# Optimization experiments

Measured on AMD Instinct MI355X. Metric: run time of the kernel, lower is better.

Reference implementation:

```python
import jax, jax.numpy as jnp
import numpy as np

N_NODES = 100000
N_EDGES = 1600000
F_IN = 128
H = 128
L = 3
BN_EPS = 1e-5
NORM_EPS = 1e-12


def setup_inputs() -> dict:
    key = jax.random.key(0)
    ks = jax.random.split(key, 32)
    def rn(k, shape, s=0.05):
        return jax.random.normal(k, shape, dtype=jnp.float32) * s
    inp = {
        'x': jax.random.normal(ks[0], (N_NODES, F_IN), dtype=jnp.float32),
        'edge_index': jax.random.randint(ks[1], (2, N_EDGES), 0, N_NODES, dtype=jnp.int32),
        # node encoder
        'enc_w': rn(ks[2], (H, F_IN)), 'enc_b': rn(ks[3], (H,)),
        # per-layer SAGEConv params (stacked over layers)
        'lin_l_w': rn(ks[4], (L, H, H)), 'lin_l_b': rn(ks[5], (L, H)),
        'lin_r_w': rn(ks[6], (L, H, H)),
        # batch norms (eval mode: running stats)
        'bn_gamma': jnp.ones((L, H), jnp.float32), 'bn_beta': jnp.zeros((L, H), jnp.float32),
        'bn_mean': jnp.zeros((L, H), jnp.float32), 'bn_var': jnp.ones((L, H), jnp.float32),
        # output head
        'out_w1': rn(ks[7], (H, H)), 'out_b1': rn(ks[8], (H,)),
        'out_w2': rn(ks[9], (1, H)), 'out_b2': rn(ks[10], (1,)),
        # cost head
        'cost_w1': rn(ks[11], (H // 2, H)), 'cost_b1': rn(ks[12], (H // 2,)),
        'cost_w2': rn(ks[13], (1, H // 2)), 'cost_b2': rn(ks[14], (1,)),
        # bullwhip head
        'bw_w1': rn(ks[15], (H // 2, H)), 'bw_b1': rn(ks[16], (H // 2,)),
        'bw_w2': rn(ks[17], (1, H // 2)), 'bw_b2': rn(ks[18], (1,)),
    }
    return inp


def _sage_conv(h, src, dst, wl, bl, wr):
    # PyG SAGEConv (aggr='mean', normalize=True): lin_l(mean_j x_j) + lin_r(x_i), then L2 normalize
    msg_sum = jax.ops.segment_sum(h[src], dst, num_segments=N_NODES)  # [N, H]
    deg = jax.ops.segment_sum(jnp.ones((src.shape[0],), h.dtype), dst, num_segments=N_NODES)
    mean = msg_sum / jnp.maximum(deg, 1.0)[:, None]
    out = mean @ wl.T + bl + h @ wr.T
    norm = jnp.linalg.norm(out, axis=-1, keepdims=True)
    return out / jnp.maximum(norm, NORM_EPS)


def reference(x, edge_index, enc_w, enc_b, lin_l_w, lin_l_b, lin_r_w,
              bn_gamma, bn_beta, bn_mean, bn_var,
              out_w1, out_b1, out_w2, out_b2,
              cost_w1, cost_b1, cost_w2, cost_b2,
              bw_w1, bw_b1, bw_w2, bw_b2):
    src, dst = edge_index[0], edge_index[1]
    h = jax.nn.relu(x @ enc_w.T + enc_b)  # dropout is identity in eval
    for i in range(L):
        h = _sage_conv(h, src, dst, lin_l_w[i], lin_l_b[i], lin_r_w[i])
        # BatchNorm1d in eval mode
        h = (h - bn_mean[i]) * (bn_gamma[i] / jnp.sqrt(bn_var[i] + BN_EPS)) + bn_beta[i]
        h = jax.nn.relu(h)
    order = jax.nn.relu(h @ out_w1.T + out_b1) @ out_w2.T + out_b2
    cost = jax.nn.relu(h @ cost_w1.T + cost_b1) @ cost_w2.T + cost_b2
    bullwhip = jax.nn.relu(h @ bw_w1.T + bw_b1) @ bw_w2.T + bw_b2
    return (order, cost, bullwhip, h)
```

## Files before the change

### kernel.cpp

```cpp
#include <hip/hip_runtime.h>

#define NN 100000
#define NE 1600000
#define TN 16
#define TNL 32
#define NBK 391
#define BCAP 5120
#define CTILE 8192

static constexpr float BN_EPS = 1e-5f;
static constexpr float NORM_EPS = 1e-12f;

typedef unsigned int u32;
typedef unsigned short u16;
typedef __attribute__((ext_vector_type(8))) short short8;
typedef __attribute__((ext_vector_type(4))) float f32x4;

__device__ __forceinline__ float bflo(u32 u) {
    u32 v = u << 16; float f; __builtin_memcpy(&f, &v, 4); return f;
}
__device__ __forceinline__ float bfhi(u32 u) {
    u32 v = u & 0xffff0000u; float f; __builtin_memcpy(&f, &v, 4); return f;
}
__device__ __forceinline__ u32 packbf(float a, float b) {
    u32 ua, ub; __builtin_memcpy(&ua, &a, 4); __builtin_memcpy(&ub, &b, 4);
    u32 ra = (ua + 0x7fffu + ((ua >> 16) & 1u)) >> 16;
    u32 rb = (ub + 0x7fffu + ((ub >> 16) & 1u)) & 0xffff0000u;
    return ra | rb;
}
__device__ __forceinline__ u16 f2bf(float a) {
    u32 ua; __builtin_memcpy(&ua, &a, 4);
    return (u16)((ua + 0x7fffu + ((ua >> 16) & 1u)) >> 16);
}
__device__ __forceinline__ void acc8(float* s, uint4 v) {
    s[0] += bflo(v.x); s[1] += bfhi(v.x);
    s[2] += bflo(v.y); s[3] += bfhi(v.y);
    s[4] += bflo(v.z); s[5] += bfhi(v.z);
    s[6] += bflo(v.w); s[7] += bfhi(v.w);
}
__device__ __forceinline__ f32x4 mfma16(uint4 a, uint4 b, f32x4 c) {
    return __builtin_amdgcn_mfma_f32_16x16x32_bf16(
        __builtin_bit_cast(short8, a), __builtin_bit_cast(short8, b), c, 0, 0, 0);
}

struct TposeArgs {
    const float* src[10];
    u16* dst[10];
    int rows[10];
};

__global__ void frag_kernel(TposeArgs a) {
    const int m = blockIdx.x;
    const float* __restrict__ s = a.src[m];
    u16* __restrict__ d = a.dst[m];
    const int total = a.rows[m] * 128;
    for (int idx = threadIdx.x; idx < total; idx += 256) {
        const int i = idx & 7;
        const int l = (idx >> 3) & 63;
        const int kk = (idx >> 9) & 3;
        const int jt = idx >> 11;
        const int j = jt * 16 + (l & 15);
        const int k = kk * 32 + ((l >> 4) << 3) + i;
        d[idx] = f2bf(s[j * 128 + k]);
    }
}

__global__ __launch_bounds__(256, 4)
void bucket_scatter_kernel(const int* __restrict__ e_src, const int* __restrict__ e_dst,
                           int* __restrict__ bcnt, u32* __restrict__ ebuf) {
    __shared__ int h[NBK];
    const int tid = threadIdx.x;
    const int base = blockIdx.x * CTILE;
    const int end = (base + CTILE < NE) ? base + CTILE : NE;
    for (int i = tid; i < NBK; i += 256) h[i] = 0;
    __syncthreads();
    for (int e = base + tid; e < end; e += 256)
        atomicAdd(&h[e_dst[e] >> 8], 1);
    __syncthreads();
    for (int i = tid; i < NBK; i += 256) {
        const int c = h[i];
        h[i] = (c > 0) ? atomicAdd(&bcnt[i], c) : 0;
    }
    __syncthreads();
    for (int e = base + tid; e < end; e += 256) {
        const int d = e_dst[e];
        const int b = d >> 8;
        const int slot = atomicAdd(&h[b], 1);
        if (slot < BCAP)
            ebuf[(size_t)b * BCAP + slot] = (u32)e_src[e] | ((u32)(d & 255) << 17);
    }
}

__global__ void bscan_kernel(const int* __restrict__ bcnt, int* __restrict__ bbase) {
    const int lane = threadIdx.x;
    const int per = (NBK + 63) / 64;
    int vals[8];
    int s = 0;
    for (int i = 0; i < per; ++i) {
        const int idx = lane * per + i;
        const int v = (idx < NBK) ? bcnt[idx] : 0;
        vals[i] = s; s += v;
    }
    int incl = s;
    for (int off = 1; off < 64; off <<= 1) {
        const int t = __shfl_up(incl, off);
        if (lane >= off) incl += t;
    }
    const int excl = incl - s;
    for (int i = 0; i < per; ++i) {
        const int idx = lane * per + i;
        if (idx < NBK) bbase[idx] = excl + vals[i];
    }
    if (lane == 63) bbase[NBK] = excl + s;
}

__global__ __launch_bounds__(256, 4)
void csr_finalize_kernel(const u32* __restrict__ ebuf, const int* __restrict__ bcnt,
                         const int* __restrict__ bbase,
                         int* __restrict__ row_ptr, float* __restrict__ inv_deg,
                         int* __restrict__ csr_src) {
    __shared__ int cnt[256];
    __shared__ int rc[256];
    const int b = blockIdx.x;
    const int tid = threadIdx.x;
    const int n0 = b << 8;
    const int nb_nodes = (NN - n0 < 256) ? NN - n0 : 256;
    int ecnt = bcnt[b];
    if (ecnt > BCAP) ecnt = BCAP;
    const int gbase = bbase[b];
    const u32* eb = ebuf + (size_t)b * BCAP;
    cnt[tid] = 0;
    __syncthreads();
    for (int e = tid; e < ecnt; e += 256)
        atomicAdd(&cnt[eb[e] >> 17], 1);
    __syncthreads();
    const int myc = cnt[tid];
    int val = myc;
    for (int off = 1; off < 256; off <<= 1) {
        const int t = (tid >= off) ? cnt[tid - off] : 0;
        __syncthreads();
        val += t;
        cnt[tid] = val;
        __syncthreads();
    }
    const int excl = val - myc;
    if (tid < nb_nodes) {
        row_ptr[n0 + tid] = gbase + excl;
        inv_deg[n0 + tid] = 1.0f / (float)(myc < 1 ? 1 : myc);
    }
    rc[tid] = gbase + excl;
    __syncthreads();
    for (int e = tid; e < ecnt; e += 256) {
        const u32 p = eb[e];
        const int pos = atomicAdd(&rc[p >> 17], 1);
        csr_src[pos] = (int)(p & 0x1FFFFu);
    }
    if (b == NBK - 1 && tid == 0) row_ptr[NN] = NE;
}

__global__ __launch_bounds__(256, 6)
void encoder_kernel(const float* __restrict__ x, u16* __restrict__ h_out,
                    const u16* __restrict__ wfrag, const float* __restrict__ bias) {
    __shared__ uint4 sRows[256];
    const int tid = threadIdx.x;
    const int nb = blockIdx.x * TN;

    {
        const int row = tid >> 4, t = tid & 15;
        const float4* xr = (const float4*)(x + (size_t)(nb + row) * 128 + t * 8);
        const float4 xa = xr[0], xb = xr[1];
        uint4 p;
        p.x = packbf(xa.x, xa.y); p.y = packbf(xa.z, xa.w);
        p.z = packbf(xb.x, xb.y); p.w = packbf(xb.z, xb.w);
        sRows[row * 16 + (t ^ (row & 7))] = p;
    }
    __syncthreads();

    const int lane = tid & 63, wave = tid >> 6;
    const int cl = lane & 15, gq = lane >> 4;
    const int jt0 = wave * 2, jt1 = wave * 2 + 1;
    const uint4* wf = (const uint4*)wfrag;
    f32x4 a0 = {0, 0, 0, 0}, a1 = {0, 0, 0, 0};
    #pragma unroll
    for (int kk = 0; kk < 4; ++kk) {
        const uint4 af = sRows[cl * 16 + ((kk * 4 + gq) ^ (cl & 7))];
        a0 = mfma16(af, wf[(jt0 * 4 + kk) * 64 + lane], a0);
        a1 = mfma16(af, wf[(jt1 * 4 + kk) * 64 + lane], a1);
    }
    const int c0 = jt0 * 16 + cl, c1 = jt1 * 16 + cl;
    const float b0 = bias[c0], b1 = bias[c1];
    __syncthreads();
    u16* st = (u16*)sRows;
    #pragma unroll
    for (int r = 0; r < 4; ++r) {
        const int rw = gq * 4 + r;
        st[rw * 128 + c0] = f2bf(fmaxf(a0[r] + b0, 0.f));
        st[rw * 128 + c1] = f2bf(fmaxf(a1[r] + b1, 0.f));
    }
    __syncthreads();
    uint4* dst = (uint4*)(h_out + (size_t)nb * 128);
    dst[tid] = ((const uint4*)st)[tid];
}

template<int LAST>
__global__ __launch_bounds__(256, 8)
void sage_layer_kernel(const u16* __restrict__ h_in,
                       u16* __restrict__ h_out_bf, float* __restrict__ o_h,
                       const u16* __restrict__ wlfrag, const float* __restrict__ bl,
                       const u16* __restrict__ wrfrag,
                       const float* __restrict__ bn_g, const float* __restrict__ bn_b,
                       const float* __restrict__ bn_m, const float* __restrict__ bn_v,
                       const int* __restrict__ row_ptr, const int* __restrict__ csr_src,
                       const float* __restrict__ inv_deg,
                       const u16* __restrict__ o1frag, const float* __restrict__ ob1,
                       const float* __restrict__ ow2, const float* __restrict__ ob2,
                       const u16* __restrict__ c1frag, const float* __restrict__ cb1,
                       const float* __restrict__ cw2, const float* __restrict__ cb2,
                       const u16* __restrict__ b1frag, const float* __restrict__ bb1,
                       const float* __restrict__ bw2, const float* __restrict__ bb2,
                       float* __restrict__ o_order, float* __restrict__ o_cost,
                       float* __restrict__ o_bw) {
    __shared__ uint4 sRows[512];
    __shared__ uint4 sMean[512];
    __shared__ float ssb[4][32];
    const int tid = threadIdx.x;
    const int nb = blockIdx.x * TNL;

    {
        const uint4* src = (const uint4*)h_in + (size_t)nb * 16;
        const int i0 = tid, i1 = tid + 256;
        sRows[(i0 >> 4) * 16 + ((i0 & 15) ^ ((i0 >> 4) & 7))] = src[i0];
        sRows[(i1 >> 4) * 16 + ((i1 & 15) ^ ((i1 >> 4) & 7))] = src[i1];
    }

    {
        const int g = tid >> 4, t = tid & 15;
        const uint4* hb = (const uint4*)h_in;
        #pragma unroll
        for (int half = 0; half < 2; ++half) {
            const int row = g + half * 16;
            const int n = nb + row;
            float acc[8] = {0, 0, 0, 0, 0, 0, 0, 0};
            const int rp0 = row_ptr[n], rp1 = row_ptr[n + 1];
            int e = rp0;
            for (; e + 3 < rp1; e += 4) {
                const int s0 = csr_src[e], s1 = csr_src[e + 1];
                const int s2 = csr_src[e + 2], s3 = csr_src[e + 3];
                const uint4 va = hb[(size_t)s0 * 16 + t];
                const uint4 vb = hb[(size_t)s1 * 16 + t];
                const uint4 vc = hb[(size_t)s2 * 16 + t];
                const uint4 vd = hb[(size_t)s3 * 16 + t];
                acc8(acc, va); acc8(acc, vb); acc8(acc, vc); acc8(acc, vd);
            }
            for (; e < rp1; ++e) acc8(acc, hb[(size_t)csr_src[e] * 16 + t]);
            const float id = inv_deg[n];
            uint4 mp;
            mp.x = packbf(acc[0] * id, acc[1] * id);
            mp.y = packbf(acc[2] * id, acc[3] * id);
            mp.z = packbf(acc[4] * id, acc[5] * id);
            mp.w = packbf(acc[6] * id, acc[7] * id);
            sMean[row * 16 + (t ^ (row & 7))] = mp;
        }
    }
    __syncthreads();

    const int lane = tid & 63, wave = tid >> 6;
    const int cl = lane & 15, gq = lane >> 4;
    const int jt0 = wave * 2, jt1 = wave * 2 + 1;
    f32x4 a00 = {0,0,0,0}, a01 = {0,0,0,0}, a10 = {0,0,0,0}, a11 = {0,0,0,0};
    {
        const uint4* wf = (const uint4*)wlfrag;
        #pragma unroll
        for (int kk = 0; kk < 4; ++kk) {
            const int ch = (kk * 4 + gq) ^ (cl & 7);
            const uint4 af0 = sMean[cl * 16 + ch];
            const uint4 af1 = sMean[(16 + cl) * 16 + ch];
            const uint4 b0 = wf[(jt0 * 4 + kk) * 64 + lane];
            const uint4 b1 = wf[(jt1 * 4 + kk) * 64 + lane];
            a00 = mfma16(af0, b0, a00); a01 = mfma16(af0, b1, a01);
            a10 = mfma16(af1, b0, a10); a11 = mfma16(af1, b1, a11);
        }
    }
    {
        const uint4* wf = (const uint4*)wrfrag;
        #pragma unroll
        for (int kk = 0; kk < 4; ++kk) {
            const int ch = (kk * 4 + gq) ^ (cl & 7);
            const uint4 af0 = sRows[cl * 16 + ch];
            const uint4 af1 = sRows[(16 + cl) * 16 + ch];
            const uint4 b0 = wf[(jt0 * 4 + kk) * 64 + lane];
            const uint4 b1 = wf[(jt1 * 4 + kk) * 64 + lane];
            a00 = mfma16(af0, b0, a00); a01 = mfma16(af0, b1, a01);
            a10 = mfma16(af1, b0, a10); a11 = mfma16(af1, b1, a11);
        }
    }

    const int c0 = jt0 * 16 + cl, c1 = jt1 * 16 + cl;
    const float bl0 = bl[c0], bl1 = bl[c1];
    float t00[4], t01[4], t10[4], t11[4], ss0[4], ss1[4];
    #pragma unroll
    for (int r = 0; r < 4; ++r) {
        t00[r] = a00[r] + bl0; t01[r] = a01[r] + bl1;
        t10[r] = a10[r] + bl0; t11[r] = a11[r] + bl1;
        ss0[r] = t00[r] * t00[r] + t01[r] * t01[r];
        ss1[r] = t10[r] * t10[r] + t11[r] * t11[r];
    }
    #pragma unroll
    for (int m = 1; m <= 8; m <<= 1) {
        #pragma unroll
        for (int r = 0; r < 4; ++r) {
            ss0[r] += __shfl_xor(ss0[r], m);
            ss1[r] += __shfl_xor(ss1[r], m);
        }
    }
    if (cl == 0) {
        #pragma unroll
        for (int r = 0; r < 4; ++r) {
            ssb[wave][gq * 4 + r] = ss0[r];
            ssb[wave][16 + gq * 4 + r] = ss1[r];
        }
    }
    __syncthreads();

    const float sc0 = bn_g[c0] * rsqrtf(bn_v[c0] + BN_EPS);
    const float sc1 = bn_g[c1] * rsqrtf(bn_v[c1] + BN_EPS);
    const float m0 = bn_m[c0], m1 = bn_m[c1];
    const float bb0 = bn_b[c0], bb1v = bn_b[c1];
    float f00[4], f01[4], f10[4], f11[4];
    #pragma unroll
    for (int r = 0; r < 4; ++r) {
        const int rw0 = gq * 4 + r, rw1 = 16 + rw0;
        const float tot0 = ssb[0][rw0] + ssb[1][rw0] + ssb[2][rw0] + ssb[3][rw0];
        const float tot1 = ssb[0][rw1] + ssb[1][rw1] + ssb[2][rw1] + ssb[3][rw1];
        const float inv0 = 1.0f / fmaxf(sqrtf(tot0), NORM_EPS);
        const float inv1 = 1.0f / fmaxf(sqrtf(tot1), NORM_EPS);
        f00[r] = fmaxf((t00[r] * inv0 - m0) * sc0 + bb0, 0.f);
        f01[r] = fmaxf((t01[r] * inv0 - m1) * sc1 + bb1v, 0.f);
        f10[r] = fmaxf((t10[r] * inv1 - m0) * sc0 + bb0, 0.f);
        f11[r] = fmaxf((t11[r] * inv1 - m1) * sc1 + bb1v, 0.f);
    }

    if (!LAST) {
        u16* st = (u16*)sMean;
        #pragma unroll
        for (int r = 0; r < 4; ++r) {
            const int rw0 = gq * 4 + r, rw1 = 16 + rw0;
            st[rw0 * 128 + c0] = f2bf(f00[r]);
            st[rw0 * 128 + c1] = f2bf(f01[r]);
            st[rw1 * 128 + c0] = f2bf(f10[r]);
            st[rw1 * 128 + c1] = f2bf(f11[r]);
        }
        __syncthreads();
        uint4* dst = (uint4*)(h_out_bf + (size_t)nb * 128);
        dst[tid] = ((const uint4*)st)[tid];
        dst[tid + 256] = ((const uint4*)st)[tid + 256];
        return;
    }

    {
        float* stf = (float*)sMean;
        #pragma unroll
        for (int r = 0; r < 4; ++r) {
            const int rw0 = gq * 4 + r;
            stf[rw0 * 128 + c0] = f00[r];
            stf[rw0 * 128 + c1] = f01[r];
        }
        __syncthreads();
        float4* dst0 = (float4*)(o_h + (size_t)nb * 128);
        dst0[tid] = ((const float4*)stf)[tid];
        dst0[tid + 256] = ((const float4*)stf)[tid + 256];
        __syncthreads();
        #pragma unroll
        for (int r = 0; r < 4; ++r) {
            const int rw0 = gq * 4 + r;
            stf[rw0 * 128 + c0] = f10[r];
            stf[rw0 * 128 + c1] = f11[r];
        }
        __syncthreads();
        float4* dst1 = (float4*)(o_h + (size_t)(nb + 16) * 128);
        dst1[tid] = ((const float4*)stf)[tid];
        dst1[tid + 256] = ((const float4*)stf)[tid + 256];
    }

    u16* sr16 = (u16*)sRows;
    #pragma unroll
    for (int r = 0; r < 4; ++r) {
        const int rw0 = gq * 4 + r, rw1 = 16 + rw0;
        sr16[rw0 * 128 + (((c0 >> 3) ^ (rw0 & 7)) << 3) + (c0 & 7)] = f2bf(f00[r]);
        sr16[rw0 * 128 + (((c1 >> 3) ^ (rw0 & 7)) << 3) + (c1 & 7)] = f2bf(f01[r]);
        sr16[rw1 * 128 + (((c0 >> 3) ^ (rw1 & 7)) << 3) + (c0 & 7)] = f2bf(f10[r]);
        sr16[rw1 * 128 + (((c1 >> 3) ^ (rw1 & 7)) << 3) + (c1 & 7)] = f2bf(f11[r]);
    }
    __syncthreads();

    {
        const uint4* wf = (const uint4*)o1frag;
        f32x4 h00 = {0,0,0,0}, h01 = {0,0,0,0}, h10 = {0,0,0,0}, h11 = {0,0,0,0};
        #pragma unroll
        for (int kk = 0; kk < 4; ++kk) {
            const int ch = (kk * 4 + gq) ^ (cl & 7);
            const uint4 af0 = sRows[cl * 16 + ch];
            const uint4 af1 = sRows[(16 + cl) * 16 + ch];
            const uint4 b0 = wf[(jt0 * 4 + kk) * 64 + lane];
            const uint4 b1 = wf[(jt1 * 4 + kk) * 64 + lane];
            h00 = mfma16(af0, b0, h00); h01 = mfma16(af0, b1, h01);
            h10 = mfma16(af1, b0, h10); h11 = mfma16(af1, b1, h11);
        }
        const float hb0 = ob1[c0], hb1 = ob1[c1];
        const float w20 = ow2[c0], w21 = ow2[c1];
        float p0[4], p1[4];
        #pragma unroll
        for (int r = 0; r < 4; ++r) {
            p0[r] = fmaxf(h00[r] + hb0, 0.f) * w20 + fmaxf(h01[r] + hb1, 0.f) * w21;
            p1[r] = fmaxf(h10[r] + hb0, 0.f) * w20 + fmaxf(h11[r] + hb1, 0.f) * w21;
        }
        #pragma unroll
        for (int m = 1; m <= 8; m <<= 1) {
            #pragma unroll
            for (int r = 0; r < 4; ++r) {
                p0[r] += __shfl_xor(p0[r], m);
                p1[r] += __shfl_xor(p1[r], m);
            }
        }
        if (cl == 0) {
            #pragma unroll
            for (int r = 0; r < 4; ++r) {
                ssb[wave][gq * 4 + r] = p0[r];
                ssb[wave][16 + gq * 4 + r] = p1[r];
            }
        }
        __syncthreads();
        if (tid < 32)
            o_order[nb + tid] = ssb[0][tid] + ssb[1][tid] + ssb[2][tid] + ssb[3][tid] + ob2[0];
        __syncthreads();
    }

    const u16* hfr[2] = {c1frag, b1frag};
    const float* hb1a[2] = {cb1, bb1};
    const float* hw2a[2] = {cw2, bw2};
    const float* hb2a[2] = {cb2, bb2};
    float* outs[2] = {o_cost, o_bw};
    #pragma unroll
    for (int ph = 0; ph < 2; ++ph) {
        const uint4* wf = (const uint4*)hfr[ph];
        f32x4 g0 = {0,0,0,0}, g1 = {0,0,0,0};
        #pragma unroll
        for (int kk = 0; kk < 4; ++kk) {
            const int ch = (kk * 4 + gq) ^ (cl & 7);
            const uint4 af0 = sRows[cl * 16 + ch];
            const uint4 af1 = sRows[(16 + cl) * 16 + ch];
            const uint4 b = wf[(wave * 4 + kk) * 64 + lane];
            g0 = mfma16(af0, b, g0);
            g1 = mfma16(af1, b, g1);
        }
        const int cc = wave * 16 + cl;
        const float hb = hb1a[ph][cc], w2 = hw2a[ph][cc];
        float p0[4], p1[4];
        #pragma unroll
        for (int r = 0; r < 4; ++r) {
            p0[r] = fmaxf(g0[r] + hb, 0.f) * w2;
            p1[r] = fmaxf(g1[r] + hb, 0.f) * w2;
        }
        #pragma unroll
        for (int m = 1; m <= 8; m <<= 1) {
            #pragma unroll
            for (int r = 0; r < 4; ++r) {
                p0[r] += __shfl_xor(p0[r], m);
                p1[r] += __shfl_xor(p1[r], m);
            }
        }
        if (cl == 0) {
            #pragma unroll
            for (int r = 0; r < 4; ++r) {
                ssb[wave][gq * 4 + r] = p0[r];
                ssb[wave][16 + gq * 4 + r] = p1[r];
            }
        }
        __syncthreads();
        if (tid < 32)
            outs[ph][nb + tid] = ssb[0][tid] + ssb[1][tid] + ssb[2][tid] + ssb[3][tid] + hb2a[ph][0];
        __syncthreads();
    }
}

extern "C" void kernel_launch(void* const* d_in, const int* in_sizes, int n_in,
                              void* d_out, int out_size, void* d_ws, size_t ws_size,
                              hipStream_t stream) {
    (void)in_sizes; (void)n_in; (void)out_size;

    const float* x       = (const float*)d_in[0];
    const int*   ei      = (const int*)d_in[1];
    const float* enc_w   = (const float*)d_in[2];
    const float* enc_b   = (const float*)d_in[3];
    const float* ll_w    = (const float*)d_in[4];
    const float* ll_b    = (const float*)d_in[5];
    const float* lr_w    = (const float*)d_in[6];
    const float* bn_g    = (const float*)d_in[7];
    const float* bn_b    = (const float*)d_in[8];
    const float* bn_m    = (const float*)d_in[9];
    const float* bn_v    = (const float*)d_in[10];
    const float* out_w1  = (const float*)d_in[11];
    const float* out_b1  = (const float*)d_in[12];
    const float* out_w2  = (const float*)d_in[13];
    const float* out_b2  = (const float*)d_in[14];
    const float* cost_w1 = (const float*)d_in[15];
    const float* cost_b1 = (const float*)d_in[16];
    const float* cost_w2 = (const float*)d_in[17];
    const float* cost_b2 = (const float*)d_in[18];
    const float* bw_w1   = (const float*)d_in[19];
    const float* bw_b1   = (const float*)d_in[20];
    const float* bw_w2   = (const float*)d_in[21];
    const float* bw_b2   = (const float*)d_in[22];

    const int* e_src = ei;
    const int* e_dst = ei + NE;

    float* o_order = (float*)d_out;
    float* o_cost  = o_order + NN;
    float* o_bw    = o_cost + NN;
    float* o_h     = o_bw + NN;

    u16* hA = (u16*)d_ws;
    u16* hB = hA + (size_t)NN * 128;
    u16* wt = hB + (size_t)NN * 128;
    u16* wt_enc  = wt;
    u16* wt_ll   = wt + 16384;
    u16* wt_lr   = wt + 16384 * 4;
    u16* wt_out1 = wt + 16384 * 7;
    u16* wt_c1   = wt + 16384 * 8;
    u16* wt_bw1  = wt + 16384 * 8 + 8192;
    int* row_ptr  = (int*)(wt + 147456);
    float* inv_deg = (float*)(row_ptr + NN + 4);
    int* csr_src  = (int*)(inv_deg + NN);
    int* bcnt     = csr_src + NE;
    int* bbase    = bcnt + NBK + 1;
    u32* ebuf     = (u32*)(bbase + NBK + 1);

    const size_t need = (size_t)((char*)(ebuf + (size_t)NBK * BCAP) - (char*)d_ws);
    if (ws_size < need) return;

    (void)hipMemsetAsync(bcnt, 0, (NBK + 1) * sizeof(int), stream);

    TposeArgs ta;
    ta.src[0] = enc_w;          ta.dst[0] = wt_enc;          ta.rows[0] = 128;
    ta.src[1] = ll_w;           ta.dst[1] = wt_ll;           ta.rows[1] = 128;
    ta.src[2] = ll_w + 16384;   ta.dst[2] = wt_ll + 16384;   ta.rows[2] = 128;
    ta.src[3] = ll_w + 32768;   ta.dst[3] = wt_ll + 32768;   ta.rows[3] = 128;
    ta.src[4] = lr_w;           ta.dst[4] = wt_lr;           ta.rows[4] = 128;
    ta.src[5] = lr_w + 16384;   ta.dst[5] = wt_lr + 16384;   ta.rows[5] = 128;
    ta.src[6] = lr_w + 32768;   ta.dst[6] = wt_lr + 32768;   ta.rows[6] = 128;
    ta.src[7] = out_w1;         ta.dst[7] = wt_out1;         ta.rows[7] = 128;
    ta.src[8] = cost_w1;        ta.dst[8] = wt_c1;           ta.rows[8] = 64;
    ta.src[9] = bw_w1;          ta.dst[9] = wt_bw1;          ta.rows[9] = 64;
    frag_kernel<<<10, 256, 0, stream>>>(ta);

    bucket_scatter_kernel<<<(NE + CTILE - 1) / CTILE, 256, 0, stream>>>(e_src, e_dst, bcnt, ebuf);
    bscan_kernel<<<1, 64, 0, stream>>>(bcnt, bbase);
    csr_finalize_kernel<<<NBK, 256, 0, stream>>>(ebuf, bcnt, bbase, row_ptr, inv_deg, csr_src);

    encoder_kernel<<<NN / TN, 256, 0, stream>>>(x, hA, wt_enc, enc_b);
    sage_layer_kernel<0><<<NN / TNL, 256, 0, stream>>>(hA, hB, nullptr, wt_ll, ll_b, wt_lr,
        bn_g, bn_b, bn_m, bn_v, row_ptr, csr_src, inv_deg,
        nullptr, nullptr, nullptr, nullptr, nullptr, nullptr, nullptr, nullptr,
        nullptr, nullptr, nullptr, nullptr, nullptr, nullptr, nullptr);
    sage_layer_kernel<0><<<NN / TNL, 256, 0, stream>>>(hB, hA, nullptr, wt_ll + 16384, ll_b + 128, wt_lr + 16384,
        bn_g + 128, bn_b + 128, bn_m + 128, bn_v + 128, row_ptr, csr_src, inv_deg,
        nullptr, nullptr, nullptr, nullptr, nullptr, nullptr, nullptr, nullptr,
        nullptr, nullptr, nullptr, nullptr, nullptr, nullptr, nullptr);
    sage_layer_kernel<1><<<NN / TNL, 256, 0, stream>>>(hA, nullptr, o_h, wt_ll + 32768, ll_b + 256, wt_lr + 32768,
        bn_g + 256, bn_b + 256, bn_m + 256, bn_v + 256, row_ptr, csr_src, inv_deg,
        wt_out1, out_b1, out_w2, out_b2,
        wt_c1, cost_b1, cost_w2, cost_b2,
        wt_bw1, bw_b1, bw_w2, bw_b2,
        o_order, o_cost, o_bw);
}
```

Measured before the change: 312.4 us.

## Split neighbor gather into column-group kernel with column-major feature layout

Node features are stored in a column-group-major layout (8 groups of 16 bf16 columns per node), and the neighbor mean aggregation moves into a separate gather kernel. Each block of that kernel handles one column group for 32 nodes, with 4 lanes splitting each node's edges and a shuffle reduction at the end. The intent is that each column-group slab (about 3.2 MB) stays cache-resident during random gathers, improving L2 hit rate. In exchange, the mean tensor makes an extra round trip through global memory, and there are three more kernel launches.

```diff
diff --git a/kernel.cpp b/kernel.cpp
--- a/kernel.cpp
+++ b/kernel.cpp
@@ -159,7 +159,7 @@
 }
 
 __global__ __launch_bounds__(256, 6)
-void encoder_kernel(const float* __restrict__ x, u16* __restrict__ h_out,
+void encoder_kernel(const float* __restrict__ x, u16* __restrict__ h_cm,
                     const u16* __restrict__ wfrag, const float* __restrict__ bias) {
     __shared__ uint4 sRows[256];
     const int tid = threadIdx.x;
@@ -194,32 +194,74 @@
     #pragma unroll
     for (int r = 0; r < 4; ++r) {
         const int rw = gq * 4 + r;
-        st[rw * 128 + c0] = f2bf(fmaxf(a0[r] + b0, 0.f));
-        st[rw * 128 + c1] = f2bf(fmaxf(a1[r] + b1, 0.f));
-    }
-    __syncthreads();
-    uint4* dst = (uint4*)(h_out + (size_t)nb * 128);
-    dst[tid] = ((const uint4*)st)[tid];
+        st[rw * 128 + (((c0 >> 3) ^ (rw & 7)) << 3) + (c0 & 7)] = f2bf(fmaxf(a0[r] + b0, 0.f));
+        st[rw * 128 + (((c1 >> 3) ^ (rw & 7)) << 3) + (c1 & 7)] = f2bf(fmaxf(a1[r] + b1, 0.f));
+    }
+    __syncthreads();
+    {
+        const int cg = tid >> 5, r = (tid >> 1) & 15, hf = tid & 1;
+        const int chunk = cg * 2 + hf;
+        ((uint4*)h_cm)[((size_t)cg * NN + nb + r) * 2 + hf] =
+            sRows[r * 16 + (chunk ^ (r & 7))];
+    }
+}
+
+__global__ __launch_bounds__(256, 8)
+void gather_cm_kernel(const u16* __restrict__ h_cm, u16* __restrict__ mean_cm,
+                      const int* __restrict__ row_ptr, const int* __restrict__ csr_src,
+                      const float* __restrict__ inv_deg) {
+    const int cg = blockIdx.x & 7;
+    const int nb = (blockIdx.x >> 3) * 32;
+    const int t = threadIdx.x;
+    const int g = t >> 3;
+    const int sub = t & 7;
+    const int es = sub >> 1;
+    const int hf = sub & 1;
+    const int n = nb + g;
+    const uint4* hb = (const uint4*)h_cm + (size_t)cg * NN * 2;
+    float acc[8] = {0, 0, 0, 0, 0, 0, 0, 0};
+    const int rp0 = row_ptr[n], rp1 = row_ptr[n + 1];
+    int e = rp0 + es;
+    for (; e + 4 < rp1; e += 8) {
+        const int s0 = csr_src[e];
+        const int s1 = csr_src[e + 4];
+        const uint4 v0 = hb[(size_t)s0 * 2 + hf];
+        const uint4 v1 = hb[(size_t)s1 * 2 + hf];
+        acc8(acc, v0); acc8(acc, v1);
+    }
+    if (e < rp1) acc8(acc, hb[(size_t)csr_src[e] * 2 + hf]);
+    #pragma unroll
+    for (int i = 0; i < 8; ++i) {
+        acc[i] += __shfl_xor(acc[i], 2);
+        acc[i] += __shfl_xor(acc[i], 4);
+    }
+    if (es == 0) {
+        const float id = inv_deg[n];
+        uint4 mp;
+        mp.x = packbf(acc[0] * id, acc[1] * id);
+        mp.y = packbf(acc[2] * id, acc[3] * id);
+        mp.z = packbf(acc[4] * id, acc[5] * id);
+        mp.w = packbf(acc[6] * id, acc[7] * id);
+        ((uint4*)mean_cm)[((size_t)cg * NN + n) * 2 + hf] = mp;
+    }
 }
 
 template<int LAST>
 __global__ __launch_bounds__(256, 8)
-void sage_layer_kernel(const u16* __restrict__ h_in,
-                       u16* __restrict__ h_out_bf, float* __restrict__ o_h,
-                       const u16* __restrict__ wlfrag, const float* __restrict__ bl,
-                       const u16* __restrict__ wrfrag,
-                       const float* __restrict__ bn_g, const float* __restrict__ bn_b,
-                       const float* __restrict__ bn_m, const float* __restrict__ bn_v,
-                       const int* __restrict__ row_ptr, const int* __restrict__ csr_src,
-                       const float* __restrict__ inv_deg,
-                       const u16* __restrict__ o1frag, const float* __restrict__ ob1,
-                       const float* __restrict__ ow2, const float* __restrict__ ob2,
-                       const u16* __restrict__ c1frag, const float* __restrict__ cb1,
-                       const float* __restrict__ cw2, const float* __restrict__ cb2,
-                       const u16* __restrict__ b1frag, const float* __restrict__ bb1,
-                       const float* __restrict__ bw2, const float* __restrict__ bb2,
-                       float* __restrict__ o_order, float* __restrict__ o_cost,
-                       float* __restrict__ o_bw) {
+void sage_mm_kernel(const u16* __restrict__ h_cm, const u16* __restrict__ mean_cm,
+                    u16* __restrict__ hout_cm, float* __restrict__ o_h,
+                    const u16* __restrict__ wlfrag, const float* __restrict__ bl,
+                    const u16* __restrict__ wrfrag,
+                    const float* __restrict__ bn_g, const float* __restrict__ bn_b,
+                    const float* __restrict__ bn_m, const float* __restrict__ bn_v,
+                    const u16* __restrict__ o1frag, const float* __restrict__ ob1,
+                    const float* __restrict__ ow2, const float* __restrict__ ob2,
+                    const u16* __restrict__ c1frag, const float* __restrict__ cb1,
+                    const float* __restrict__ cw2, const float* __restrict__ cb2,
+                    const u16* __restrict__ b1frag, const float* __restrict__ bb1,
+                    const float* __restrict__ bw2, const float* __restrict__ bb2,
+                    float* __restrict__ o_order, float* __restrict__ o_cost,
+                    float* __restrict__ o_bw) {
     __shared__ uint4 sRows[512];
     __shared__ uint4 sMean[512];
     __shared__ float ssb[4][32];
@@ -227,39 +269,17 @@
     const int nb = blockIdx.x * TNL;
 
     {
-        const uint4* src = (const uint4*)h_in + (size_t)nb * 16;
-        const int i0 = tid, i1 = tid + 256;
-        sRows[(i0 >> 4) * 16 + ((i0 & 15) ^ ((i0 >> 4) & 7))] = src[i0];
-        sRows[(i1 >> 4) * 16 + ((i1 & 15) ^ ((i1 >> 4) & 7))] = src[i1];
-    }
-
-    {
-        const int g = tid >> 4, t = tid & 15;
-        const uint4* hb = (const uint4*)h_in;
-        #pragma unroll
-        for (int half = 0; half < 2; ++half) {
-            const int row = g + half * 16;
-            const int n = nb + row;
-            float acc[8] = {0, 0, 0, 0, 0, 0, 0, 0};
-            const int rp0 = row_ptr[n], rp1 = row_ptr[n + 1];
-            int e = rp0;
-            for (; e + 3 < rp1; e += 4) {
-                const int s0 = csr_src[e], s1 = csr_src[e + 1];
-                const int s2 = csr_src[e + 2], s3 = csr_src[e + 3];
-                const uint4 va = hb[(size_t)s0 * 16 + t];
-                const uint4 vb = hb[(size_t)s1 * 16 + t];
-                const uint4 vc = hb[(size_t)s2 * 16 + t];
-                const uint4 vd = hb[(size_t)s3 * 16 + t];
-                acc8(acc, va); acc8(acc, vb); acc8(acc, vc); acc8(acc, vd);
-            }
-            for (; e < rp1; ++e) acc8(acc, hb[(size_t)csr_src[e] * 16 + t]);
-            const float id = inv_deg[n];
-            uint4 mp;
-            mp.x = packbf(acc[0] * id, acc[1] * id);
-            mp.y = packbf(acc[2] * id, acc[3] * id);
-            mp.z = packbf(acc[4] * id, acc[5] * id);
-            mp.w = packbf(acc[6] * id, acc[7] * id);
-            sMean[row * 16 + (t ^ (row & 7))] = mp;
+        const uint4* hs = (const uint4*)h_cm;
+        const uint4* ms = (const uint4*)mean_cm;
+        #pragma unroll
+        for (int p = 0; p < 2; ++p) {
+            const int i = tid + p * 256;
+            const int cg = i >> 6, r = (i >> 1) & 31, hf = i & 1;
+            const int chunk = cg * 2 + hf;
+            const size_t gidx = ((size_t)cg * NN + nb + r) * 2 + hf;
+            const int lidx = r * 16 + (chunk ^ (r & 7));
+            sRows[lidx] = hs[gidx];
+            sMean[lidx] = ms[gidx];
         }
     }
     __syncthreads();
@@ -345,15 +365,20 @@
         #pragma unroll
         for (int r = 0; r < 4; ++r) {
             const int rw0 = gq * 4 + r, rw1 = 16 + rw0;
-            st[rw0 * 128 + c0] = f2bf(f00[r]);
-            st[rw0 * 128 + c1] = f2bf(f01[r]);
-            st[rw1 * 128 + c0] = f2bf(f10[r]);
-            st[rw1 * 128 + c1] = f2bf(f11[r]);
-        }
-        __syncthreads();
-        uint4* dst = (uint4*)(h_out_bf + (size_t)nb * 128);
-        dst[tid] = ((const uint4*)st)[tid];
-        dst[tid + 256] = ((const uint4*)st)[tid + 256];
+            st[rw0 * 128 + (((c0 >> 3) ^ (rw0 & 7)) << 3) + (c0 & 7)] = f2bf(f00[r]);
+            st[rw0 * 128 + (((c1 >> 3) ^ (rw0 & 7)) << 3) + (c1 & 7)] = f2bf(f01[r]);
+            st[rw1 * 128 + (((c0 >> 3) ^ (rw1 & 7)) << 3) + (c0 & 7)] = f2bf(f10[r]);
+            st[rw1 * 128 + (((c1 >> 3) ^ (rw1 & 7)) << 3) + (c1 & 7)] = f2bf(f11[r]);
+        }
+        __syncthreads();
+        uint4* dst = (uint4*)hout_cm;
+        #pragma unroll
+        for (int p = 0; p < 2; ++p) {
+            const int i = tid + p * 256;
+            const int cg = i >> 6, r = (i >> 1) & 31, hf = i & 1;
+            const int chunk = cg * 2 + hf;
+            dst[((size_t)cg * NN + nb + r) * 2 + hf] = sMean[r * 16 + (chunk ^ (r & 7))];
+        }
         return;
     }
 
@@ -520,9 +545,10 @@
     float* o_bw    = o_cost + NN;
     float* o_h     = o_bw + NN;
 
-    u16* hA = (u16*)d_ws;
-    u16* hB = hA + (size_t)NN * 128;
-    u16* wt = hB + (size_t)NN * 128;
+    u16* hA      = (u16*)d_ws;
+    u16* hB      = hA + (size_t)NN * 128;
+    u16* mean_cm = hB + (size_t)NN * 128;
+    u16* wt      = mean_cm + (size_t)NN * 128;
     u16* wt_enc  = wt;
     u16* wt_ll   = wt + 16384;
     u16* wt_lr   = wt + 16384 * 4;
@@ -558,17 +584,26 @@
     bscan_kernel<<<1, 64, 0, stream>>>(bcnt, bbase);
     csr_finalize_kernel<<<NBK, 256, 0, stream>>>(ebuf, bcnt, bbase, row_ptr, inv_deg, csr_src);
 
+    const int NG = (NN / TNL) * 8;
     encoder_kernel<<<NN / TN, 256, 0, stream>>>(x, hA, wt_enc, enc_b);
-    sage_layer_kernel<0><<<NN / TNL, 256, 0, stream>>>(hA, hB, nullptr, wt_ll, ll_b, wt_lr,
-        bn_g, bn_b, bn_m, bn_v, row_ptr, csr_src, inv_deg,
+
+    gather_cm_kernel<<<NG, 256, 0, stream>>>(hA, mean_cm, row_ptr, csr_src, inv_deg);
+    sage_mm_kernel<0><<<NN / TNL, 256, 0, stream>>>(hA, mean_cm, hB, nullptr,
+        wt_ll, ll_b, wt_lr, bn_g, bn_b, bn_m, bn_v,
         nullptr, nullptr, nullptr, nullptr, nullptr, nullptr, nullptr, nullptr,
         nullptr, nullptr, nullptr, nullptr, nullptr, nullptr, nullptr);
-    sage_layer_kernel<0><<<NN / TNL, 256, 0, stream>>>(hB, hA, nullptr, wt_ll + 16384, ll_b + 128, wt_lr + 16384,
-        bn_g + 128, bn_b + 128, bn_m + 128, bn_v + 128, row_ptr, csr_src, inv_deg,
+
+    gather_cm_kernel<<<NG, 256, 0, stream>>>(hB, mean_cm, row_ptr, csr_src, inv_deg);
+    sage_mm_kernel<0><<<NN / TNL, 256, 0, stream>>>(hB, mean_cm, hA, nullptr,
+        wt_ll + 16384, ll_b + 128, wt_lr + 16384,
+        bn_g + 128, bn_b + 128, bn_m + 128, bn_v + 128,
         nullptr, nullptr, nullptr, nullptr, nullptr, nullptr, nullptr, nullptr,
         nullptr, nullptr, nullptr, nullptr, nullptr, nullptr, nullptr);
-    sage_layer_kernel<1><<<NN / TNL, 256, 0, stream>>>(hA, nullptr, o_h, wt_ll + 32768, ll_b + 256, wt_lr + 32768,
-        bn_g + 256, bn_b + 256, bn_m + 256, bn_v + 256, row_ptr, csr_src, inv_deg,
+
+    gather_cm_kernel<<<NG, 256, 0, stream>>>(hA, mean_cm, row_ptr, csr_src, inv_deg);
+    sage_mm_kernel<1><<<NN / TNL, 256, 0, stream>>>(hA, mean_cm, nullptr, o_h,
+        wt_ll + 32768, ll_b + 256, wt_lr + 32768,
+        bn_g + 256, bn_b + 256, bn_m + 256, bn_v + 256,
         wt_out1, out_b1, out_w2, out_b2,
         wt_c1, cost_b1, cost_w2, cost_b2,
         wt_bw1, bw_b1, bw_w2, bw_b2,
```

Result: slower. 386.3 us (+23.7%).
